# Kernel tuning notes

Measured on AMD Instinct MI355X. Metric: run time of the kernel, lower is better.

## Reference

```python
import jax, jax.numpy as jnp
import numpy as np

B, T, F, U, M = 4096, 16, 256, 512, 8
DELTA_T = 0.04

# ln_tau_table: tau = 1, 10^0.5, 10^1.0, ... -> ln(tau) = i * 0.5*ln(10)
LN_TAU = (jnp.arange(M, dtype=jnp.float32) * (0.5 * np.log(10.0))).astype(jnp.float32)
DECAY = jnp.exp(-DELTA_T / (LN_TAU + 1e-7))  # [M]


def setup_inputs() -> dict:
    key = jax.random.key(0)
    ks = jax.random.split(key, 9)
    s = lambda fan_in: 1.0 / np.sqrt(fan_in)
    return {
        "x": jax.random.normal(ks[0], (B, T, F), dtype=jnp.float32),
        "W_r": jax.random.normal(ks[1], (F + U, U * M), dtype=jnp.float32) * s(F + U),
        "b_r": jax.random.normal(ks[2], (U * M,), dtype=jnp.float32) * 0.01,
        "W_q": jax.random.normal(ks[3], (F + U, U), dtype=jnp.float32) * s(F + U),
        "b_q": jax.random.normal(ks[4], (U,), dtype=jnp.float32) * 0.01,
        "W_s": jax.random.normal(ks[5], (F + U, U * M), dtype=jnp.float32) * s(F + U),
        "b_s": jax.random.normal(ks[6], (U * M,), dtype=jnp.float32) * 0.01,
        "W_out": jax.random.normal(ks[7], (U, 3), dtype=jnp.float32) * s(U),
        "b_out": jax.random.normal(ks[8], (3,), dtype=jnp.float32) * 0.01,
    }


def _ctgru_forward(x, W_r, b_r, W_q, b_q, W_s, b_s, W_out, b_out):
    def step(h_hat, x_t):  # h_hat: [B,U,M], x_t: [B,F]
        h = h_hat.sum(axis=2)                              # [B,U]
        fused = jnp.concatenate([x_t, h], axis=1)          # [B,F+U]
        ln_tau_r = (fused @ W_r + b_r).reshape(-1, U, M)   # [B,U,M]
        r_ki = jax.nn.softmax(-jnp.square(ln_tau_r - LN_TAU), axis=2)
        q_in = jnp.concatenate([x_t, jnp.sum(r_ki * h_hat, axis=2)], axis=1)
        q_k = jnp.tanh(q_in @ W_q + b_q)[:, :, None]       # [B,U,1]
        ln_tau_s = (fused @ W_s + b_s).reshape(-1, U, M)
        s_ki = jax.nn.softmax(-jnp.square(ln_tau_s - LN_TAU), axis=2)
        h_next = ((1.0 - s_ki) * h_hat + s_ki * q_k) * DECAY
        return h_next, h_next.sum(axis=2)                  # carry, hidden [B,U]

    h0 = jnp.zeros((x.shape[0], U, M), dtype=x.dtype)
    _, hiddens = jax.lax.scan(step, h0, jnp.swapaxes(x, 0, 1))  # hiddens: [T,B,U]
    outputs = jnp.swapaxes(hiddens, 0, 1)                  # [B,T,U]
    return outputs @ W_out + b_out                         # [B,T,3]


def reference(x, W_r, b_r, W_q, b_q, W_s, b_s, W_out, b_out):
    return _ctgru_forward(x, W_r, b_r, W_q, b_q, W_s, b_s, W_out, b_out)
```

## Files before the change

### kernel.cpp

```cpp
#include <hip/hip_runtime.h>
#include <hip/hip_bf16.h>
#include <math.h>

#define B_   4096
#define T_   16
#define F_   256
#define U_   512
#define M_   8
#define K_   768
#define NRS  4096
#define NC   8192
#define LNT  1.1512925f

typedef __bf16 bf16_t;
typedef bf16_t bf16x8 __attribute__((ext_vector_type(8)));
typedef bf16_t bf16x4 __attribute__((ext_vector_type(4)));
typedef float  f32x4  __attribute__((ext_vector_type(4)));

__device__ inline void gl_lds16(const void* g, void* lds) {
    __builtin_amdgcn_global_load_lds(
        (const __attribute__((address_space(1))) unsigned int*)g,
        (__attribute__((address_space(3))) unsigned int*)lds, 16, 0, 0);
}

#define VMCNT(n) asm volatile("s_waitcnt vmcnt(" #n ")" ::: "memory")
#define LGKM0()  asm volatile("s_waitcnt lgkmcnt(0)" ::: "memory")
#define BAR()    __builtin_amdgcn_s_barrier()

__device__ inline void stage_ht(const bf16_t* src, bf16_t* dst, int tid) {
    gl_lds16(src + tid * 8,        (char*)dst + tid * 16);
    gl_lds16(src + tid * 8 + 4096, (char*)dst + tid * 16 + 8192);
}

__global__ __launch_bounds__(512, 1) void gemm_rs_v8(
    const bf16_t* __restrict__ xt_t,
    const bf16_t* __restrict__ ht,
    const bf16_t* __restrict__ Bt,
    const float*  __restrict__ biasP,
    const bf16_t* __restrict__ hhat,
    bf16_t* __restrict__ rh,
    bf16_t* __restrict__ sbuf)
{
    __shared__ __attribute__((aligned(16))) bf16_t Ah[2][2][8192];
    __shared__ __attribute__((aligned(16))) bf16_t Bh[2][2][8192];

    const int tid  = threadIdx.x;
    const int lane = tid & 63;
    const int wave = tid >> 6;

    const int lin = blockIdx.y * 16 + blockIdx.x;
    const int xcd = lin & 7, q = lin >> 3;
    const int m0 = ((xcd >> 1) * 4 + (q & 3)) * 256;
    const int n0 = ((xcd & 1) * 16 + (q >> 2)) * 256;
    const int mp = m0 >> 8, np = n0 >> 8;

    const int wm = wave >> 2;
    const int wn = wave & 3;
    const int lr = lane & 15;
    const int kq = lane >> 4;
    const int ck0 = (kq ^ (lr & 7)) * 8;

    const bf16_t* Ab0 = &Ah[0][wm][0] + lr * 64;
    const bf16_t* Ab1 = &Ah[1][wm][0] + lr * 64;
    const bf16_t* Bb0 = &Bh[0][wn >> 1][0] + ((wn & 1) * 64 + lr) * 64;
    const bf16_t* Bb1 = &Bh[1][wn >> 1][0] + ((wn & 1) * 64 + lr) * 64;

    f32x4 acc[8][4] = {};
    bf16x8 a[8], b[8];

#define AS(T, H) ((T) < 4 ? xt_t + ((size_t)(mp * 4 + (T)) * 2 + (H)) * 8192  \
                          : ht  + ((size_t)(mp * 8 + (T) - 4) * 2 + (H)) * 8192)
#define BS(T, H) (Bt + ((size_t)(np * 12 + (T)) * 2 + (H)) * 8192)

#define RDA(P, mh) do{ const bf16_t* _p = (P) + (mh) * 4096;                   \
    a[0]=*(const bf16x8*)(_p+ck0);      a[1]=*(const bf16x8*)(_p+(ck0^32));    \
    a[2]=*(const bf16x8*)(_p+1024+ck0); a[3]=*(const bf16x8*)(_p+1024+(ck0^32)); \
    a[4]=*(const bf16x8*)(_p+2048+ck0); a[5]=*(const bf16x8*)(_p+2048+(ck0^32)); \
    a[6]=*(const bf16x8*)(_p+3072+ck0); a[7]=*(const bf16x8*)(_p+3072+(ck0^32)); }while(0)

#define RDB(P, nh) do{ const bf16_t* _p = (P) + (nh) * 2048;                   \
    b[(nh)*4+0]=*(const bf16x8*)(_p+ck0);                                      \
    b[(nh)*4+1]=*(const bf16x8*)(_p+(ck0^32));                                 \
    b[(nh)*4+2]=*(const bf16x8*)(_p+1024+ck0);                                 \
    b[(nh)*4+3]=*(const bf16x8*)(_p+1024+(ck0^32)); }while(0)

#define MMA(MH, NH) do{ __builtin_amdgcn_s_setprio(1);                         \
    _Pragma("unroll") for (int ai = 0; ai < 4; ++ai)                           \
      _Pragma("unroll") for (int bj = 0; bj < 2; ++bj)                         \
        acc[(MH)*4+ai][(NH)*2+bj] = __builtin_amdgcn_mfma_f32_16x16x32_bf16(   \
            a[ai*2+0], b[(NH)*4+bj*2+0], acc[(MH)*4+ai][(NH)*2+bj], 0, 0, 0);  \
    _Pragma("unroll") for (int ai = 0; ai < 4; ++ai)                           \
      _Pragma("unroll") for (int bj = 0; bj < 2; ++bj)                         \
        acc[(MH)*4+ai][(NH)*2+bj] = __builtin_amdgcn_mfma_f32_16x16x32_bf16(   \
            a[ai*2+1], b[(NH)*4+bj*2+1], acc[(MH)*4+ai][(NH)*2+bj], 0, 0, 0);  \
    __builtin_amdgcn_s_setprio(0); }while(0)

    stage_ht(AS(0, 0), &Ah[0][0][0], tid);
    stage_ht(AS(0, 1), &Ah[0][1][0], tid);
    stage_ht(BS(0, 0), &Bh[0][0][0], tid);
    stage_ht(BS(0, 1), &Bh[0][1][0], tid);
    stage_ht(AS(1, 0), &Ah[1][0][0], tid);
    stage_ht(AS(1, 1), &Ah[1][1][0], tid);
    stage_ht(BS(1, 0), &Bh[1][0][0], tid);
    stage_ht(BS(1, 1), &Bh[1][1][0], tid);
    VMCNT(8);
    BAR();

#define ITER_S(E) do{                                                          \
    RDA(Ab0,0); RDB(Bb0,0);                    BAR(); LGKM0(); MMA(0,0); BAR();\
    RDB(Bb0,1);                                BAR(); LGKM0(); MMA(0,1); BAR();\
    RDA(Ab0,1); stage_ht(BS((E)+2,0), &Bh[0][0][0], tid);                      \
                                               BAR(); LGKM0(); MMA(1,1); BAR();\
    stage_ht(BS((E)+2,1), &Bh[0][1][0], tid);                                  \
                                    BAR(); LGKM0(); MMA(1,0); VMCNT(4); BAR(); \
    RDA(Ab1,0); RDB(Bb1,0); stage_ht(AS((E)+2,0), &Ah[0][0][0], tid);          \
                                               BAR(); LGKM0(); MMA(0,0); BAR();\
    RDB(Bb1,1); stage_ht(AS((E)+2,1), &Ah[0][1][0], tid);                      \
                                               BAR(); LGKM0(); MMA(0,1); BAR();\
    RDA(Ab1,1); stage_ht(BS((E)+3,0), &Bh[1][0][0], tid);                      \
                                               BAR(); LGKM0(); MMA(1,1); BAR();\
    stage_ht(BS((E)+3,1), &Bh[1][1][0], tid);                                  \
    stage_ht(AS((E)+3,0), &Ah[1][0][0], tid);                                  \
    stage_ht(AS((E)+3,1), &Ah[1][1][0], tid);                                  \
                                    BAR(); LGKM0(); MMA(1,0); VMCNT(8); BAR(); \
}while(0)

#define ITER_L() do{                                                           \
    RDA(Ab0,0); RDB(Bb0,0);                    BAR(); LGKM0(); MMA(0,0); BAR();\
    RDB(Bb0,1);                                BAR(); LGKM0(); MMA(0,1); BAR();\
    RDA(Ab0,1);                                BAR(); LGKM0(); MMA(1,1); BAR();\
                                    BAR(); LGKM0(); MMA(1,0); VMCNT(0); BAR(); \
    RDA(Ab1,0); RDB(Bb1,0);                    BAR(); LGKM0(); MMA(0,0); BAR();\
    RDB(Bb1,1);                                BAR(); LGKM0(); MMA(0,1); BAR();\
    RDA(Ab1,1);                                BAR(); LGKM0(); MMA(1,1); BAR();\
                                               BAR(); LGKM0(); MMA(1,0);       \
}while(0)

    ITER_S(0);
    ITER_S(2);
    ITER_S(4);
    ITER_S(6);
    ITER_S(8);
    ITER_L();

#undef ITER_S
#undef ITER_L
#undef MMA
#undef RDA
#undef RDB
#undef AS
#undef BS

    const int nb  = n0 + wn * 64;
    const int u3  = lane & 7;
    const int m0v = ((lane >> 3) & 1) * 4;
    const bool is_r = nb < NRS;

    float bj4[4];
#pragma unroll
    for (int j = 0; j < 4; ++j) bj4[j] = biasP[nb + j * 16 + lr];

#pragma unroll
    for (int mi = 0; mi < 8; ++mi) {
        const int rowb = m0 + wm * 128 + mi * 16 + kq * 4;
#pragma unroll
        for (int r = 0; r < 4; ++r) {
            const int row = rowb + r;
            float e[4], sum = 0.f;
#pragma unroll
            for (int j = 0; j < 4; ++j) {
                float v = acc[mi][j][r] + bj4[j];
                float d = v - (float)(m0v + j) * LNT;
                e[j] = __expf(-d * d);
                sum += e[j];
            }
            sum += __shfl_xor(sum, 8, 64);
            const float inv = 1.0f / sum;
            if (is_r) {
                bf16x4 h4 = *(const bf16x4*)(hhat + (size_t)row * NRS + nb + u3 * 8 + m0v);
                float rhv = 0.f;
#pragma unroll
                for (int j = 0; j < 4; ++j) rhv += e[j] * inv * (float)h4[j];
                rhv += __shfl_xor(rhv, 8, 64);
                if ((lane & 8) == 0)
                    rh[(size_t)row * U_ + (nb >> 3) + u3] = (bf16_t)rhv;
            } else {
                bf16x4 pv;
#pragma unroll
                for (int j = 0; j < 4; ++j) pv[j] = (bf16_t)(e[j] * inv);
                *(bf16x4*)(sbuf + (size_t)row * NRS + (nb - NRS) + u3 * 8 + m0v) = pv;
            }
        }
    }
}

__global__ __launch_bounds__(256) void gemm_q_up(
    const bf16_t* __restrict__ xt_t,
    const bf16_t* __restrict__ rh,
    const bf16_t* __restrict__ Bqt,
    const float*  __restrict__ bq,
    const bf16_t* __restrict__ sbuf,
    bf16_t* __restrict__ hhat,
    bf16_t* __restrict__ hnext,
    bf16_t* __restrict__ htile)
{
    __shared__ __attribute__((aligned(16))) bf16_t As[4096];
    __shared__ __attribute__((aligned(16))) bf16_t Bs[4096];

    const int tid  = threadIdx.x;
    const int lane = tid & 63;
    const int wave = tid >> 6;
    const int m0 = blockIdx.x * 64;
    const int n0 = blockIdx.y * 64;
    const int wm = wave & 1;
    const int wn = wave >> 1;
    const int lr = lane & 15;
    const int kq = lane >> 4;
    const int ck0 = (kq ^ (lr & 7)) * 8;

    const int mp = m0 >> 8, half = (m0 >> 7) & 1, r0 = m0 & 127;
    const int rw = tid >> 3, q8 = tid & 7;

    f32x4 acc[2][2] = {};

    for (int kt = 0; kt < 12; ++kt) {
        __syncthreads();
        if (kt < 4) {
            const bf16_t* s = xt_t + ((size_t)(mp * 4 + kt) * 2 + half) * 8192 + r0 * 64;
            gl_lds16(s + tid * 8,        (char*)As + tid * 16);
            gl_lds16(s + tid * 8 + 2048, (char*)As + tid * 16 + 4096);
        } else {
            const int cb = (kt - 4) * 64;
            gl_lds16(rh + (size_t)(m0 + rw) * U_ + cb + ((q8 ^ (rw & 7)) * 8),
                     (char*)As + tid * 16);
            gl_lds16(rh + (size_t)(m0 + 32 + rw) * U_ + cb + ((q8 ^ (rw & 7)) * 8),
                     (char*)As + tid * 16 + 4096);
        }
        {
            const bf16_t* s = Bqt + (size_t)((n0 >> 6) * 12 + kt) * 4096;
            gl_lds16(s + tid * 8,        (char*)Bs + tid * 16);
            gl_lds16(s + tid * 8 + 2048, (char*)Bs + tid * 16 + 4096);
        }
        __syncthreads();

        bf16x8 af[4], bfr[4];
#pragma unroll
        for (int i = 0; i < 2; i++) {
            const bf16_t* pa = As + (wm * 32 + i * 16 + lr) * 64;
            const bf16_t* pb = Bs + (wn * 32 + i * 16 + lr) * 64;
            af[i * 2 + 0]  = *(const bf16x8*)(pa + ck0);
            af[i * 2 + 1]  = *(const bf16x8*)(pa + (ck0 ^ 32));
            bfr[i * 2 + 0] = *(const bf16x8*)(pb + ck0);
            bfr[i * 2 + 1] = *(const bf16x8*)(pb + (ck0 ^ 32));
        }
#pragma unroll
        for (int ks = 0; ks < 2; ks++)
#pragma unroll
            for (int i = 0; i < 2; i++)
#pragma unroll
                for (int j = 0; j < 2; j++)
                    acc[i][j] = __builtin_amdgcn_mfma_f32_16x16x32_bf16(
                        af[i * 2 + ks], bfr[j * 2 + ks], acc[i][j], 0, 0, 0);
    }

    const float DEC[8] = {0.0f, 0.9658531f, 0.9827783f, 0.9884856f,
                          0.9913518f, 0.9930754f, 0.9942261f, 0.9950489f};

#pragma unroll
    for (int i = 0; i < 2; i++) {
        const int rowb = m0 + wm * 32 + i * 16 + kq * 4;
#pragma unroll
        for (int j = 0; j < 2; j++) {
            const int u = n0 + wn * 32 + j * 16 + lr;
            const float bv = bq[u];
            const int kt2 = u >> 6, kc = u & 63;
#pragma unroll
            for (int r = 0; r < 4; r++) {
                const int row = rowb + r;
                const float qv = tanhf(acc[i][j][r] + bv);
                const size_t base = (size_t)row * NRS + u * 8;
                bf16x8 s8 = *(const bf16x8*)(sbuf + base);
                bf16x8 h8 = *(const bf16x8*)(hhat + base);
                bf16x8 ho;
                float hs = 0.f;
#pragma unroll
                for (int m = 0; m < 8; m++) {
                    float s = (float)s8[m];
                    float h = (float)h8[m];
                    float hn = ((1.f - s) * h + s * qv) * DEC[m];
                    ho[m] = (bf16_t)hn;
                    hs += hn;
                }
                *(bf16x8*)(hhat + base) = ho;
                hnext[(size_t)row * U_ + u] = (bf16_t)hs;
                htile[((((size_t)(row >> 8) * 8 + kt2) * 2 + ((row >> 7) & 1)) * 128
                       + (row & 127)) * 64
                      + (((kc >> 3) ^ (row & 7)) * 8) + (kc & 7)] = (bf16_t)hs;
            }
        }
    }
}

__global__ void transpose_perm(const float* __restrict__ src, bf16_t* __restrict__ dst) {
    __shared__ float tl[32][33];
    int k0 = blockIdx.x * 32, n0 = blockIdx.y * 32;
    int tx = threadIdx.x & 31, ty = threadIdx.x >> 5;
#pragma unroll
    for (int i = 0; i < 32; i += 8)
        tl[ty + i][tx] = src[(size_t)(k0 + ty + i) * NRS + n0 + tx];
    __syncthreads();
#pragma unroll
    for (int i = 0; i < 32; i += 8) {
        int n = n0 + ty + i;
        int m = n & 7, u3v = (n >> 3) & 7;
        int p = (n & ~63) + (m & 3) * 16 + (m >> 2) * 8 + u3v;
        dst[(size_t)p * K_ + k0 + tx] = (bf16_t)tl[tx][ty + i];
    }
}

__global__ void btile_build(const bf16_t* __restrict__ WrsT, bf16_t* __restrict__ Bt) {
    int n = blockIdx.x / 3;
    int k = (blockIdx.x % 3) * 256 + threadIdx.x;
    int np = n >> 8, rp = n & 255, hf = rp >> 7, r = rp & 127;
    int kt = k >> 6, kc = k & 63;
    Bt[((((size_t)np * 12 + kt) * 2 + hf) * 128 + r) * 64
       + (((kc >> 3) ^ (r & 7)) * 8) + (kc & 7)] = WrsT[(size_t)n * K_ + k];
}

__global__ void transpose_plain(const float* __restrict__ src, bf16_t* __restrict__ dst, int N) {
    __shared__ float tl[32][33];
    int k0 = blockIdx.x * 32, n0 = blockIdx.y * 32;
    int tx = threadIdx.x & 31, ty = threadIdx.x >> 5;
#pragma unroll
    for (int i = 0; i < 32; i += 8)
        tl[ty + i][tx] = src[(size_t)(k0 + ty + i) * N + n0 + tx];
    __syncthreads();
#pragma unroll
    for (int i = 0; i < 32; i += 8)
        dst[(size_t)(n0 + ty + i) * K_ + k0 + tx] = (bf16_t)tl[tx][ty + i];
}

__global__ void bqtile_build(const bf16_t* __restrict__ WqT, bf16_t* __restrict__ Bqt) {
    int n = blockIdx.x / 3;
    int k = (blockIdx.x % 3) * 256 + threadIdx.x;
    int np = n >> 6, r = n & 63;
    int kt = k >> 6, kc = k & 63;
    Bqt[(((size_t)np * 12 + kt) * 64 + r) * 64
        + (((kc >> 3) ^ (r & 7)) * 8) + (kc & 7)] = WqT[(size_t)n * K_ + k];
}

__global__ void bias_perm(const float* __restrict__ b_r, const float* __restrict__ b_s,
                          float* __restrict__ biasP) {
    int p = blockIdx.x * 256 + threadIdx.x;
    int pr = p & 63, j = pr >> 4, lr = pr & 15;
    int L = (p & ~63) + (lr & 7) * 8 + ((lr >> 3) & 1) * 4 + j;
    biasP[p] = (L < NRS) ? b_r[L] : b_s[L - NRS];
}

__global__ void xtile_build(const float* __restrict__ x, bf16_t* __restrict__ xt) {
    int idx = blockIdx.x * 256 + threadIdx.x;
    int b = idx >> 12;
    int rem = idx & 4095;
    int t = rem >> 8, f = rem & 255;
    int mp = b >> 8, rp = b & 255, hf = rp >> 7, r = rp & 127;
    int kt = f >> 6, kc = f & 63;
    xt[(((((size_t)t * 16 + mp) * 4 + kt) * 2 + hf) * 128 + r) * 64
       + (((kc >> 3) ^ (r & 7)) * 8) + (kc & 7)] = (bf16_t)x[idx];
}

__global__ __launch_bounds__(256) void out_all(
    const bf16_t* __restrict__ hall,
    const float* __restrict__ Wout,
    const float* __restrict__ bout,
    float* __restrict__ out)
{
    int row = blockIdx.x * 4 + (threadIdx.x >> 6);
    int lane = threadIdx.x & 63;
    bf16x8 h8 = *(const bf16x8*)(hall + (size_t)row * U_ + lane * 8);
    float p0 = 0, p1 = 0, p2 = 0;
#pragma unroll
    for (int k = 0; k < 8; k++) {
        float h = (float)h8[k];
        int u = lane * 8 + k;
        p0 += h * Wout[u * 3 + 0];
        p1 += h * Wout[u * 3 + 1];
        p2 += h * Wout[u * 3 + 2];
    }
    for (int off = 32; off; off >>= 1) {
        p0 += __shfl_down(p0, off, 64);
        p1 += __shfl_down(p1, off, 64);
        p2 += __shfl_down(p2, off, 64);
    }
    if (lane == 0) {
        int t = row >> 12, b = row & (B_ - 1);
        size_t o = ((size_t)b * T_ + t) * 3;
        out[o + 0] = p0 + bout[0];
        out[o + 1] = p1 + bout[1];
        out[o + 2] = p2 + bout[2];
    }
}

extern "C" void kernel_launch(void* const* d_in, const int* in_sizes, int n_in,
                              void* d_out, int out_size, void* d_ws, size_t ws_size,
                              hipStream_t stream) {
    const float* x   = (const float*)d_in[0];
    const float* W_r = (const float*)d_in[1];
    const float* b_r = (const float*)d_in[2];
    const float* W_q = (const float*)d_in[3];
    const float* b_q = (const float*)d_in[4];
    const float* W_s = (const float*)d_in[5];
    const float* b_s = (const float*)d_in[6];
    const float* W_o = (const float*)d_in[7];
    const float* b_o = (const float*)d_in[8];
    float* out = (float*)d_out;

    char* ws = (char*)d_ws;
    bf16_t* hhat  = (bf16_t*)ws; ws += (size_t)B_ * NRS * 2;
    bf16_t* sbuf  = (bf16_t*)ws; ws += (size_t)B_ * NRS * 2;
    bf16_t* xtile = (bf16_t*)ws; ws += (size_t)B_ * T_ * F_ * 2;
    bf16_t* hall  = (bf16_t*)ws; ws += (size_t)(T_ + 1) * B_ * U_ * 2;
    bf16_t* rh    = (bf16_t*)ws; ws += (size_t)B_ * U_ * 2;
    bf16_t* WrsT  = (bf16_t*)ws; ws += (size_t)NC * K_ * 2;
    bf16_t* Btile = (bf16_t*)ws; ws += (size_t)NC * K_ * 2;
    bf16_t* htile = (bf16_t*)ws; ws += (size_t)B_ * U_ * 2;
    bf16_t* WqT   = (bf16_t*)ws; ws += (size_t)U_ * K_ * 2;
    bf16_t* Bqtil = (bf16_t*)ws; ws += (size_t)U_ * K_ * 2;
    float*  biasP = (float*)ws;  ws += (size_t)NC * 4;

    hipMemsetAsync(hhat, 0, (size_t)B_ * NRS * 2, stream);
    hipMemsetAsync(htile, 0, (size_t)B_ * U_ * 2, stream);
    xtile_build<<<B_ * T_ * F_ / 256, 256, 0, stream>>>(x, xtile);
    transpose_perm<<<dim3(K_ / 32, NRS / 32), 256, 0, stream>>>(W_r, WrsT);
    transpose_perm<<<dim3(K_ / 32, NRS / 32), 256, 0, stream>>>(W_s, WrsT + (size_t)NRS * K_);
    btile_build<<<NC * 3, 256, 0, stream>>>(WrsT, Btile);
    transpose_plain<<<dim3(K_ / 32, U_ / 32), 256, 0, stream>>>(W_q, WqT, U_);
    bqtile_build<<<U_ * 3, 256, 0, stream>>>(WqT, Bqtil);
    bias_perm<<<NC / 256, 256, 0, stream>>>(b_r, b_s, biasP);

    for (int t = 0; t < T_; t++) {
        const bf16_t* xt_t = xtile + (size_t)t * 16 * 4 * 2 * 8192;
        bf16_t*       hn   = hall + (size_t)(t + 1) * B_ * U_;
        gemm_rs_v8<<<dim3(16, 32), 512, 0, stream>>>(xt_t, htile, Btile, biasP, hhat, rh, sbuf);
        gemm_q_up<<<dim3(64, 8), 256, 0, stream>>>(xt_t, rh, Bqtil, b_q, sbuf, hhat, hn, htile);
    }
    out_all<<<B_ * T_ / 4, 256, 0, stream>>>(hall + (size_t)B_ * U_, W_o, b_o, out);
}
```

Before: 1.819 ms.

## Split r/s GEMM into two 128x128-tile kernels with simpler double buffering

Replaces the single 256x256-tile, 512-thread fused r/s GEMM with a templated 128x128-tile, 256-thread kernel launched twice per step, once for the r half and once for the s half. The new kernel has a simple two-stage LDS double buffer and allows up to four blocks per CU. The aim is higher occupancy and lower register and LDS pressure per block, replacing the hand-scheduled interleaved pipeline. In exchange, operand reuse per tile drops, and each timestep gains an extra launch and a full VMCNT(0) plus barrier on every K tile.

```diff
diff --git a/kernel.cpp b/kernel.cpp
--- a/kernel.cpp
+++ b/kernel.cpp
@@ -29,10 +29,13 @@
 
 __device__ inline void stage_ht(const bf16_t* src, bf16_t* dst, int tid) {
     gl_lds16(src + tid * 8,        (char*)dst + tid * 16);
+    gl_lds16(src + tid * 8 + 2048, (char*)dst + tid * 16 + 4096);
     gl_lds16(src + tid * 8 + 4096, (char*)dst + tid * 16 + 8192);
-}
-
-__global__ __launch_bounds__(512, 1) void gemm_rs_v8(
+    gl_lds16(src + tid * 8 + 6144, (char*)dst + tid * 16 + 12288);
+}
+
+template <int IS_R>
+__global__ __launch_bounds__(256, 4) void gemm_half(
     const bf16_t* __restrict__ xt_t,
     const bf16_t* __restrict__ ht,
     const bf16_t* __restrict__ Bt,
@@ -41,128 +44,90 @@
     bf16_t* __restrict__ rh,
     bf16_t* __restrict__ sbuf)
 {
-    __shared__ __attribute__((aligned(16))) bf16_t Ah[2][2][8192];
-    __shared__ __attribute__((aligned(16))) bf16_t Bh[2][2][8192];
+    __shared__ __attribute__((aligned(16))) bf16_t Ah[2][8192];
+    __shared__ __attribute__((aligned(16))) bf16_t Bh[2][8192];
 
     const int tid  = threadIdx.x;
     const int lane = tid & 63;
     const int wave = tid >> 6;
 
-    const int lin = blockIdx.y * 16 + blockIdx.x;
-    const int xcd = lin & 7, q = lin >> 3;
-    const int m0 = ((xcd >> 1) * 4 + (q & 3)) * 256;
-    const int n0 = ((xcd & 1) * 16 + (q >> 2)) * 256;
-    const int mp = m0 >> 8, np = n0 >> 8;
-
-    const int wm = wave >> 2;
-    const int wn = wave & 3;
+    const int lin = blockIdx.y * 32 + blockIdx.x;
+    const int c = lin & 7, q = lin >> 3;
+    const int mh = (c >> 1) * 8 + (q & 7);
+    const int nh = (c & 1) * 16 + (q >> 3);
+    const int m0 = mh * 128;
+    const int NH = IS_R ? nh : 32 + nh;
+    const int np = NH >> 1, nph = NH & 1;
+
+    const int wm = wave >> 1;
+    const int wn = wave & 1;
     const int lr = lane & 15;
     const int kq = lane >> 4;
     const int ck0 = (kq ^ (lr & 7)) * 8;
 
-    const bf16_t* Ab0 = &Ah[0][wm][0] + lr * 64;
-    const bf16_t* Ab1 = &Ah[1][wm][0] + lr * 64;
-    const bf16_t* Bb0 = &Bh[0][wn >> 1][0] + ((wn & 1) * 64 + lr) * 64;
-    const bf16_t* Bb1 = &Bh[1][wn >> 1][0] + ((wn & 1) * 64 + lr) * 64;
-
-    f32x4 acc[8][4] = {};
-    bf16x8 a[8], b[8];
-
-#define AS(T, H) ((T) < 4 ? xt_t + ((size_t)(mp * 4 + (T)) * 2 + (H)) * 8192  \
-                          : ht  + ((size_t)(mp * 8 + (T) - 4) * 2 + (H)) * 8192)
-#define BS(T, H) (Bt + ((size_t)(np * 12 + (T)) * 2 + (H)) * 8192)
-
-#define RDA(P, mh) do{ const bf16_t* _p = (P) + (mh) * 4096;                   \
-    a[0]=*(const bf16x8*)(_p+ck0);      a[1]=*(const bf16x8*)(_p+(ck0^32));    \
-    a[2]=*(const bf16x8*)(_p+1024+ck0); a[3]=*(const bf16x8*)(_p+1024+(ck0^32)); \
-    a[4]=*(const bf16x8*)(_p+2048+ck0); a[5]=*(const bf16x8*)(_p+2048+(ck0^32)); \
-    a[6]=*(const bf16x8*)(_p+3072+ck0); a[7]=*(const bf16x8*)(_p+3072+(ck0^32)); }while(0)
-
-#define RDB(P, nh) do{ const bf16_t* _p = (P) + (nh) * 2048;                   \
-    b[(nh)*4+0]=*(const bf16x8*)(_p+ck0);                                      \
-    b[(nh)*4+1]=*(const bf16x8*)(_p+(ck0^32));                                 \
-    b[(nh)*4+2]=*(const bf16x8*)(_p+1024+ck0);                                 \
-    b[(nh)*4+3]=*(const bf16x8*)(_p+1024+(ck0^32)); }while(0)
-
-#define MMA(MH, NH) do{ __builtin_amdgcn_s_setprio(1);                         \
-    _Pragma("unroll") for (int ai = 0; ai < 4; ++ai)                           \
-      _Pragma("unroll") for (int bj = 0; bj < 2; ++bj)                         \
-        acc[(MH)*4+ai][(NH)*2+bj] = __builtin_amdgcn_mfma_f32_16x16x32_bf16(   \
-            a[ai*2+0], b[(NH)*4+bj*2+0], acc[(MH)*4+ai][(NH)*2+bj], 0, 0, 0);  \
-    _Pragma("unroll") for (int ai = 0; ai < 4; ++ai)                           \
-      _Pragma("unroll") for (int bj = 0; bj < 2; ++bj)                         \
-        acc[(MH)*4+ai][(NH)*2+bj] = __builtin_amdgcn_mfma_f32_16x16x32_bf16(   \
-            a[ai*2+1], b[(NH)*4+bj*2+1], acc[(MH)*4+ai][(NH)*2+bj], 0, 0, 0);  \
+    f32x4 acc[4][4] = {};
+    bf16x8 a[4], b[4];
+
+#define AS(T) ((T) < 4 ? xt_t + ((size_t)((mh >> 1) * 4 + (T)) * 2 + (mh & 1)) * 8192 \
+                        : ht  + ((size_t)((mh >> 1) * 8 + (T) - 4) * 2 + (mh & 1)) * 8192)
+#define BS(T) (Bt + ((size_t)(np * 12 + (T)) * 2 + nph) * 8192)
+
+#define RD(dst, base, ks) do{                                                  \
+    _Pragma("unroll") for (int i = 0; i < 4; ++i)                              \
+        dst[i] = *(const bf16x8*)((base) + (i * 16 + lr) * 64 + (ck0 ^ ((ks) * 32))); \
+  }while(0)
+
+#define MMA() do{ __builtin_amdgcn_s_setprio(1);                               \
+    _Pragma("unroll") for (int i = 0; i < 4; ++i)                              \
+      _Pragma("unroll") for (int j = 0; j < 4; ++j)                            \
+        acc[i][j] = __builtin_amdgcn_mfma_f32_16x16x32_bf16(                   \
+            a[i], b[j], acc[i][j], 0, 0, 0);                                   \
     __builtin_amdgcn_s_setprio(0); }while(0)
 
-    stage_ht(AS(0, 0), &Ah[0][0][0], tid);
-    stage_ht(AS(0, 1), &Ah[0][1][0], tid);
-    stage_ht(BS(0, 0), &Bh[0][0][0], tid);
-    stage_ht(BS(0, 1), &Bh[0][1][0], tid);
-    stage_ht(AS(1, 0), &Ah[1][0][0], tid);
-    stage_ht(AS(1, 1), &Ah[1][1][0], tid);
-    stage_ht(BS(1, 0), &Bh[1][0][0], tid);
-    stage_ht(BS(1, 1), &Bh[1][1][0], tid);
-    VMCNT(8);
+    stage_ht(AS(0), &Ah[0][0], tid);
+    stage_ht(BS(0), &Bh[0][0], tid);
+    VMCNT(0);
     BAR();
 
-#define ITER_S(E) do{                                                          \
-    RDA(Ab0,0); RDB(Bb0,0);                    BAR(); LGKM0(); MMA(0,0); BAR();\
-    RDB(Bb0,1);                                BAR(); LGKM0(); MMA(0,1); BAR();\
-    RDA(Ab0,1); stage_ht(BS((E)+2,0), &Bh[0][0][0], tid);                      \
-                                               BAR(); LGKM0(); MMA(1,1); BAR();\
-    stage_ht(BS((E)+2,1), &Bh[0][1][0], tid);                                  \
-                                    BAR(); LGKM0(); MMA(1,0); VMCNT(4); BAR(); \
-    RDA(Ab1,0); RDB(Bb1,0); stage_ht(AS((E)+2,0), &Ah[0][0][0], tid);          \
-                                               BAR(); LGKM0(); MMA(0,0); BAR();\
-    RDB(Bb1,1); stage_ht(AS((E)+2,1), &Ah[0][1][0], tid);                      \
-                                               BAR(); LGKM0(); MMA(0,1); BAR();\
-    RDA(Ab1,1); stage_ht(BS((E)+3,0), &Bh[1][0][0], tid);                      \
-                                               BAR(); LGKM0(); MMA(1,1); BAR();\
-    stage_ht(BS((E)+3,1), &Bh[1][1][0], tid);                                  \
-    stage_ht(AS((E)+3,0), &Ah[1][0][0], tid);                                  \
-    stage_ht(AS((E)+3,1), &Ah[1][1][0], tid);                                  \
-                                    BAR(); LGKM0(); MMA(1,0); VMCNT(8); BAR(); \
-}while(0)
-
-#define ITER_L() do{                                                           \
-    RDA(Ab0,0); RDB(Bb0,0);                    BAR(); LGKM0(); MMA(0,0); BAR();\
-    RDB(Bb0,1);                                BAR(); LGKM0(); MMA(0,1); BAR();\
-    RDA(Ab0,1);                                BAR(); LGKM0(); MMA(1,1); BAR();\
-                                    BAR(); LGKM0(); MMA(1,0); VMCNT(0); BAR(); \
-    RDA(Ab1,0); RDB(Bb1,0);                    BAR(); LGKM0(); MMA(0,0); BAR();\
-    RDB(Bb1,1);                                BAR(); LGKM0(); MMA(0,1); BAR();\
-    RDA(Ab1,1);                                BAR(); LGKM0(); MMA(1,1); BAR();\
-                                               BAR(); LGKM0(); MMA(1,0);       \
-}while(0)
-
-    ITER_S(0);
-    ITER_S(2);
-    ITER_S(4);
-    ITER_S(6);
-    ITER_S(8);
-    ITER_L();
-
-#undef ITER_S
-#undef ITER_L
+#define TILE(T, SFLAG)                                                         \
+  {                                                                            \
+    const int p_ = (T) & 1, pn_ = p_ ^ 1;                                      \
+    if (SFLAG) {                                                               \
+      stage_ht(AS((T) + 1), &Ah[pn_][0], tid);                                 \
+      stage_ht(BS((T) + 1), &Bh[pn_][0], tid);                                 \
+    }                                                                          \
+    const bf16_t* Ab = &Ah[p_][0] + wm * 64 * 64;                              \
+    const bf16_t* Bb = &Bh[p_][0] + wn * 64 * 64;                              \
+    RD(a, Ab, 0); RD(b, Bb, 0);                                                \
+    LGKM0();                                                                   \
+    MMA();                                                                     \
+    RD(a, Ab, 1); RD(b, Bb, 1);                                                \
+    LGKM0();                                                                   \
+    MMA();                                                                     \
+    VMCNT(0);                                                                  \
+    BAR();                                                                     \
+  }
+
+    TILE(0, 1);  TILE(1, 1);  TILE(2, 1);  TILE(3, 1);
+    TILE(4, 1);  TILE(5, 1);  TILE(6, 1);  TILE(7, 1);
+    TILE(8, 1);  TILE(9, 1);  TILE(10, 1); TILE(11, 0);
+#undef TILE
 #undef MMA
-#undef RDA
-#undef RDB
+#undef RD
 #undef AS
 #undef BS
 
-    const int nb  = n0 + wn * 64;
+    const int nb  = NH * 128 + wn * 64;
     const int u3  = lane & 7;
     const int m0v = ((lane >> 3) & 1) * 4;
-    const bool is_r = nb < NRS;
 
     float bj4[4];
 #pragma unroll
     for (int j = 0; j < 4; ++j) bj4[j] = biasP[nb + j * 16 + lr];
 
 #pragma unroll
-    for (int mi = 0; mi < 8; ++mi) {
-        const int rowb = m0 + wm * 128 + mi * 16 + kq * 4;
+    for (int mi = 0; mi < 4; ++mi) {
+        const int rowb = m0 + wm * 64 + mi * 16 + kq * 4;
 #pragma unroll
         for (int r = 0; r < 4; ++r) {
             const int row = rowb + r;
@@ -176,7 +141,7 @@
             }
             sum += __shfl_xor(sum, 8, 64);
             const float inv = 1.0f / sum;
-            if (is_r) {
+            if (IS_R) {
                 bf16x4 h4 = *(const bf16x4*)(hhat + (size_t)row * NRS + nb + u3 * 8 + m0v);
                 float rhv = 0.f;
 #pragma unroll
@@ -440,7 +405,8 @@
     for (int t = 0; t < T_; t++) {
         const bf16_t* xt_t = xtile + (size_t)t * 16 * 4 * 2 * 8192;
         bf16_t*       hn   = hall + (size_t)(t + 1) * B_ * U_;
-        gemm_rs_v8<<<dim3(16, 32), 512, 0, stream>>>(xt_t, htile, Btile, biasP, hhat, rh, sbuf);
+        gemm_half<1><<<dim3(32, 32), 256, 0, stream>>>(xt_t, htile, Btile, biasP, hhat, rh, sbuf);
+        gemm_half<0><<<dim3(32, 32), 256, 0, stream>>>(xt_t, htile, Btile, biasP, hhat, rh, sbuf);
         gemm_q_up<<<dim3(64, 8), 256, 0, stream>>>(xt_t, rh, Bqtil, b_q, sbuf, hhat, hn, htile);
     }
     out_all<<<B_ * T_ / 4, 256, 0, stream>>>(hall + (size_t)B_ * U_, W_o, b_o, out);
```

Measured after the change: 1.753 ms. 1.04x faster.
